# Kernel optimization log

Hardware: AMD Instinct MI355X
Metric: run time of the kernel (lower is better)

Reference implementation:

```python
import jax, jax.numpy as jnp
import numpy as np

H = 4                      # num_heads hard-coded in SDHGNN
NAMES = ["self", "cross", "self", "cross"]
POOL_SIZES = [2, 2, 2, 2]
MIN_NGHS = 128             # minium_nghs
EPS = 1e-3                 # InstanceNorm1d eps


def _pw(x, W, b):
    # pointwise Conv1d(kernel=1): [B, Cin, N] -> [B, Cout, N]
    return jnp.einsum('oi,bin->bon', W, x) + b[None, :, None]


def _instnorm(x):
    # InstanceNorm1d (no affine): normalize over N per (B, C)
    m = jnp.mean(x, axis=2, keepdims=True)
    v = jnp.mean((x - m) ** 2, axis=2, keepdims=True)
    return (x - m) * jax.lax.rsqrt(v + EPS)


def _attn_prop(x, src, p):
    # SharedAttentionalPropagation (sharing_attention=False):
    # MultiHeadedAttention + concat + MLP residual update.
    Wq, bq, Wk, bk, Wv, bv, Wm, bm, W1, b1, W2, b2 = p
    B, D, N = x.shape
    dh = D // H
    q = _pw(x, Wq, bq).reshape(B, dh, H, N)
    k = _pw(src, Wk, bk).reshape(B, dh, H, -1)
    v = _pw(src, Wv, bv).reshape(B, dh, H, -1)
    scores = jnp.einsum('bdhn,bdhm->bhnm', q, k) * (dh ** -0.5)
    prob = jax.nn.softmax(scores, axis=-1)                     # [B,H,N,M]
    msg = jnp.einsum('bhnm,bdhm->bdhn', prob, v).reshape(B, D, N)
    msg = _pw(msg, Wm, bm)
    y = jnp.concatenate([x, msg], axis=1)                      # [B,2D,N]
    h = jax.nn.relu(_instnorm(_pw(y, W1, b1)))
    return x + _pw(h, W2, b2), prob


def _gather(x, idx):
    # x: [B,D,N], idx: [B,K] -> [B,D,K]
    return jnp.take_along_axis(
        x, jnp.broadcast_to(idx[:, None, :], (x.shape[0], x.shape[1], idx.shape[1])), axis=2)


def _pool(prob, idx, pool_size):
    # pooling_by_prob (4-D prob branch): mean over heads, sum over queries,
    # top-k by importance, sorted indices, gather global indexes.
    K = idx.shape[1]
    p = prob.mean(axis=1).sum(axis=1)                          # [B,K]
    k = min(max(K // pool_size, MIN_NGHS), K)
    _, top = jax.lax.top_k(p, k)
    top = jnp.sort(top, axis=1)
    return jnp.take_along_axis(idx, top, axis=1)


def setup_inputs() -> dict:
    key = jax.random.key(0)
    B, D, N, L = 2, 128, 2048, 4
    ks = jax.random.split(key, 16)
    s = lambda fan: 1.0 / np.sqrt(fan)
    inp = {
        'x0': jax.random.normal(ks[0], (B, D, N), jnp.float32),
        'x1': jax.random.normal(ks[1], (B, D, N), jnp.float32),
        'Wq': jax.random.normal(ks[2], (L, D, D), jnp.float32) * s(D),
        'bq': jax.random.normal(ks[3], (L, D), jnp.float32) * 0.01,
        'Wk': jax.random.normal(ks[4], (L, D, D), jnp.float32) * s(D),
        'bk': jax.random.normal(ks[5], (L, D), jnp.float32) * 0.01,
        'Wv': jax.random.normal(ks[6], (L, D, D), jnp.float32) * s(D),
        'bv': jax.random.normal(ks[7], (L, D), jnp.float32) * 0.01,
        'Wm': jax.random.normal(ks[8], (L, D, D), jnp.float32) * s(D),
        'bm': jax.random.normal(ks[9], (L, D), jnp.float32) * 0.01,
        'W1': jax.random.normal(ks[10], (L, 2 * D, 2 * D), jnp.float32) * s(2 * D),
        'b1': jax.random.normal(ks[11], (L, 2 * D), jnp.float32) * 0.01,
        'W2': jax.random.normal(ks[12], (L, D, 2 * D), jnp.float32) * s(2 * D),
        'b2': jnp.zeros((L, D), jnp.float32),  # nn.init.constant_(mlp[-1].bias, 0)
    }
    return inp


def reference(x0, x1, Wq, bq, Wk, bk, Wv, bv, Wm, bm, W1, b1, W2, b2):
    B, D, N = x0.shape
    idx0 = jnp.broadcast_to(jnp.arange(N, dtype=jnp.int32)[None], (B, N))
    idx1 = idx0
    for l, (name, ps) in enumerate(zip(NAMES, POOL_SIZES)):
        p = (Wq[l], bq[l], Wk[l], bk[l], Wv[l], bv[l],
             Wm[l], bm[l], W1[l], b1[l], W2[l], b2[l])
        if name == 'self':
            s0, s1 = _gather(x0, idx0), _gather(x1, idx1)
        else:
            s0, s1 = _gather(x1, idx1), _gather(x0, idx0)
        x0, prob0 = _attn_prop(x0, s0, p)
        x1, prob1 = _attn_prop(x1, s1, p)
        if name == 'self':
            idx0 = _pool(prob0, idx0, ps)
            idx1 = _pool(prob1, idx1, ps)
        else:
            idx1 = _pool(prob0, idx1, ps)
            idx0 = _pool(prob1, idx0, ps)
    return jnp.stack([x0, x1], axis=0)   # [2, B, D, N]
```

## Files before the change

kernel.cpp:

```cpp
#include <hip/hip_runtime.h>
#include <cstdint>
#include <cstddef>


#define NB 2
#define ND 128
#define NH 4
#define NN 2048
#define ND2 256
#define DN (ND*NN)
#define BDN (NB*DN)
#define QK_SCALE 0.2550348623f
#define IN_EPS 1e-3f

typedef unsigned short u16;
typedef __attribute__((ext_vector_type(8))) short short8;
typedef __attribute__((ext_vector_type(4))) float f32x4;

__device__ __forceinline__ u16 f2bf(float f) {
    unsigned u = __float_as_uint(f);
    return (u16)((u + 0x7fffu + ((u >> 16) & 1u)) >> 16);
}
__device__ __forceinline__ float bf2f(u16 h) {
    return __uint_as_float(((unsigned)h) << 16);
}
__device__ __forceinline__ float fexp2(float x) {
#if __has_builtin(__builtin_amdgcn_exp2f)
    return __builtin_amdgcn_exp2f(x);
#else
    return exp2f(x);
#endif
}
__device__ __forceinline__ unsigned cvtpk_bf16(float a, float b) {
    unsigned r;
    asm("v_cvt_pk_bf16_f32 %0, %1, %2" : "=v"(r) : "v"(a), "v"(b));
    return r;
}

__global__ __launch_bounds__(256) void init_kernel(
    const float* __restrict__ x0in, const float* __restrict__ x1in,
    float* __restrict__ out, int* __restrict__ idx0, int* __restrict__ idx1)
{
    int tid = blockIdx.x * 256 + threadIdx.x;
    const float4* a = (const float4*)x0in;
    const float4* b = (const float4*)x1in;
    float4* o = (float4*)out;
    o[tid] = a[tid];
    o[BDN/4 + tid] = b[tid];
    if (tid < NB*NN) {
        int v = tid & (NN-1);
        idx0[tid] = v;
        idx1[tid] = v;
    }
}

__global__ __launch_bounds__(256) void wrepack2_kernel(
    const float* __restrict__ Wq, const float* __restrict__ Wk,
    const float* __restrict__ Wv, const float* __restrict__ Wm,
    const float* __restrict__ W1, const float* __restrict__ W2,
    const float* __restrict__ bq, const float* __restrict__ bk,
    const float* __restrict__ bv,
    u16* __restrict__ whi, u16* __restrict__ wlo,
    float* __restrict__ bqp, float* __restrict__ bkp, float* __restrict__ bvp)
{
    int e = blockIdx.x * 256 + threadIdx.x;
    if (e < 655360) {
        int l = e / 163840, r = e - l*163840;
        float v;
        if (r < 49152) {
            int m = r >> 14;
            int rr = r & 16383;
            int o = rr >> 7, c = rr & 127;
            int so = (o & 31)*4 + (o >> 5);
            const float* W = (m == 0) ? Wq : ((m == 1) ? Wk : Wv);
            v = W[l*16384 + so*128 + c];
        } else if (r < 65536) {
            int rr = r - 49152;
            int o = rr >> 7, c = rr & 127;
            int sc = (c & 31)*4 + (c >> 5);
            v = Wm[l*16384 + o*128 + sc];
        } else if (r < 131072) v = W1[l*65536 + r - 65536];
        else                   v = W2[l*32768 + r - 131072];
        u16 hb = f2bf(v);
        whi[e] = hb;
        wlo[e] = f2bf(v - bf2f(hb));
    } else if (e < 656896) {
        int eb = e - 655360;
        int l = eb / 384, rr = eb % 384;
        int which = rr >> 7, o = rr & 127;
        int so = (o & 31)*4 + (o >> 5);
        float v = (which == 0 ? bq : (which == 1 ? bk : bv))[l*128 + so];
        (which == 0 ? bqp : (which == 1 ? bkp : bvp))[l*128 + o] = v;
    }
}

__global__ __launch_bounds__(256) void repack_xh_kernel(
    const float* __restrict__ in, u16* __restrict__ ohi, u16* __restrict__ olo)
{
    __shared__ float tile[32][68];
    int z = blockIdx.y >> 2, cg = blockIdx.y & 3;
    int n0 = blockIdx.x * 64;
    int t = threadIdx.x;
    {
        int i = t >> 3, nc = (t & 7) * 8;
        const float* src = &in[((size_t)z*128 + cg*32 + i)*NN + n0 + nc];
        float4 a = *(const float4*)src;
        float4 b = *(const float4*)(src + 4);
        tile[i][nc+0]=a.x; tile[i][nc+1]=a.y; tile[i][nc+2]=a.z; tile[i][nc+3]=a.w;
        tile[i][nc+4]=b.x; tile[i][nc+5]=b.y; tile[i][nc+6]=b.z; tile[i][nc+7]=b.w;
    }
    __syncthreads();
    int n = t >> 2, c8 = (t & 3) * 8;
    short8 hi, lo;
    #pragma unroll
    for (int j = 0; j < 8; ++j) {
        float v = tile[c8 + j][n];
        u16 h = f2bf(v);
        hi[j] = (short)h;
        lo[j] = (short)f2bf(v - bf2f(h));
    }
    size_t ob = ((size_t)z*NN + n0 + n)*128 + cg*32 + c8;
    *(short8*)&ohi[ob] = hi;
    *(short8*)&olo[ob] = lo;
}

__device__ __forceinline__ void gcore(
    u16* As0, u16* As1, u16* Bs0, u16* Bs1,
    const u16* __restrict__ Whi, const u16* __restrict__ Wlo, int o0, int Cin,
    const u16* __restrict__ B1hi, const u16* __restrict__ B1lo, int s1,
    const u16* __restrict__ B2hi, const u16* __restrict__ B2lo, int s2, int split,
    size_t brow, int n0, const int* __restrict__ idxp, int t, f32x4 acc[2][2])
{
    const int lane = t & 63, w = t >> 6;
    const int l15 = lane & 15, quad = lane >> 4;
    const int wr = (w & 1)*32, wc = (w >> 1)*32;
    const int ao = t >> 2, ak = (t & 3)*8;
    int grow = n0 + ao;
    if (idxp) grow = idxp[grow];
    for (int kc = 0; kc < Cin; kc += 32) {
        {
            size_t wa = (size_t)(o0 + ao)*Cin + kc + ak;
            *(short8*)&As0[ao*40 + ak] = *(const short8*)&Whi[wa];
            *(short8*)&As1[ao*40 + ak] = *(const short8*)&Wlo[wa];
        }
        {
            int c = kc + ak;
            const u16 *ph, *pl;
            size_t off;
            if (c < split) { ph = B1hi; pl = B1lo; off = (brow + grow)*s1 + c; }
            else { ph = B2hi; pl = B2lo; off = (brow + grow)*s2 + (c - split); }
            *(short8*)&Bs0[ao*40 + ak] = *(const short8*)&ph[off];
            *(short8*)&Bs1[ao*40 + ak] = *(const short8*)&pl[off];
        }
        __syncthreads();
        short8 Ah[2], Al[2], Bh[2], Bl[2];
        #pragma unroll
        for (int a = 0; a < 2; ++a) {
            Ah[a] = *(const short8*)&As0[(wr + a*16 + l15)*40 + quad*8];
            Al[a] = *(const short8*)&As1[(wr + a*16 + l15)*40 + quad*8];
        }
        #pragma unroll
        for (int c = 0; c < 2; ++c) {
            Bh[c] = *(const short8*)&Bs0[(wc + c*16 + l15)*40 + quad*8];
            Bl[c] = *(const short8*)&Bs1[(wc + c*16 + l15)*40 + quad*8];
        }
        #pragma unroll
        for (int a = 0; a < 2; ++a)
            #pragma unroll
            for (int c = 0; c < 2; ++c) {
                acc[a][c] = __builtin_amdgcn_mfma_f32_16x16x32_bf16(Ah[a], Bl[c], acc[a][c], 0,0,0);
                acc[a][c] = __builtin_amdgcn_mfma_f32_16x16x32_bf16(Al[a], Bh[c], acc[a][c], 0,0,0);
                acc[a][c] = __builtin_amdgcn_mfma_f32_16x16x32_bf16(Ah[a], Bh[c], acc[a][c], 0,0,0);
            }
        __syncthreads();
    }
}

__global__ __launch_bounds__(256) void qkv_kernel(
    const u16* __restrict__ Whi, const u16* __restrict__ Wlo,
    const float* __restrict__ bqp, const float* __restrict__ bkp,
    const float* __restrict__ bvp,
    const u16* __restrict__ xphi, const u16* __restrict__ xplo,
    const int* __restrict__ idx0, const int* __restrict__ idx1,
    int cross, int M,
    u16* __restrict__ qthi, u16* __restrict__ qtlo,
    u16* __restrict__ kthi, u16* __restrict__ ktlo,
    u16* __restrict__ vthi, float* __restrict__ p)
{
    __shared__ u16 gsm[10240];
    u16* As0 = gsm;  u16* As1 = gsm + 2560;
    u16* Bs0 = gsm + 5120; u16* Bs1 = gsm + 7680;
    float* tb = (float*)gsm;

    const int z = blockIdx.z;
    const int bx = blockIdx.x;
    const int t = threadIdx.x;
    const int lane = t & 63, w = t >> 6;
    const int l15 = lane & 15, quad = lane >> 4;
    const int wr = (w & 1)*32, wc = (w >> 1)*32;

    int role, o0, n0, nCols;
    const u16 *Wbh, *Wbl;
    const float* bias;
    if (bx < 64) {
        role = 0; o0 = (bx & 1)*64; n0 = (bx >> 1)*64; nCols = NN;
        Wbh = Whi; Wbl = Wlo; bias = bqp;
        if (t < 32) p[(size_t)z*NN + bx*32 + t] = 0.f;
    } else {
        int e = bx - 64;
        int kt = M >> 6;
        int ct = e % kt, rt = e / kt;
        n0 = ct*64; nCols = M;
        if (rt < 2) { role = 1; o0 = rt*64; Wbh = Whi+16384; Wbl = Wlo+16384; bias = bkp; }
        else        { role = 2; o0 = (rt-2)*64; Wbh = Whi+32768; Wbl = Wlo+32768; bias = bvp; }
    }
    size_t brow = (size_t)z * NN;
    const int* idxp = nullptr;
    if (role != 0) {
        int ss = cross ? 1 - (z >> 1) : (z >> 1);
        brow = (size_t)(ss*2 + (z & 1)) * NN;
        idxp = (ss ? idx1 : idx0) + (z & 1)*NN;
    }

    f32x4 acc[2][2];
    #pragma unroll
    for (int a = 0; a < 2; ++a)
        #pragma unroll
        for (int c = 0; c < 2; ++c) acc[a][c] = (f32x4){0.f,0.f,0.f,0.f};

    gcore(As0, As1, Bs0, Bs1, Wbh, Wbl, o0, 128,
          xphi, xplo, 128, xphi, xplo, 128, 128, brow, n0, idxp, t, acc);

    if (role == 2) {
        #pragma unroll
        for (int a = 0; a < 2; ++a)
            #pragma unroll
            for (int c = 0; c < 2; ++c)
                #pragma unroll
                for (int r = 0; r < 4; ++r) {
                    int row = o0 + wr + a*16 + quad*4 + r;
                    int m = n0 + wc + c*16 + l15;
                    float v = acc[a][c][r] + bias[row];
                    vthi[((size_t)(z*4 + (row>>5))*32 + (row&31))*(size_t)M + m] = f2bf(v);
                }
    } else {
        float scale = role ? 1.f : QK_SCALE;
        #pragma unroll
        for (int a = 0; a < 2; ++a)
            #pragma unroll
            for (int c = 0; c < 2; ++c)
                #pragma unroll
                for (int r = 0; r < 4; ++r) {
                    int rl = wr + a*16 + quad*4 + r;
                    tb[rl*66 + wc + c*16 + l15] = acc[a][c][r] + bias[o0 + rl];
                }
        __syncthreads();
        u16* ohi = role ? kthi : qthi;
        u16* olo = role ? ktlo : qtlo;
        int n = t >> 2, rb = (t & 3)*16;
        #pragma unroll
        for (int g = 0; g < 2; ++g) {
            short8 hi, lo;
            #pragma unroll
            for (int j = 0; j < 8; ++j) {
                float v = tb[(rb + g*8 + j)*66 + n] * scale;
                u16 hb = f2bf(v);
                hi[j] = (short)hb;
                lo[j] = (short)f2bf(v - bf2f(hb));
            }
            int rowg = o0 + rb + g*8;
            size_t ob = ((size_t)(z*4 + (rowg >> 5))*nCols + n0 + n)*32 + (rowg & 31);
            *(short8*)&ohi[ob] = hi;
            *(short8*)&olo[ob] = lo;
        }
    }
}

__global__ __launch_bounds__(512, 6) void attn4_kernel(
    const u16* __restrict__ qthi, const u16* __restrict__ qtlo,
    const u16* __restrict__ kthi, const u16* __restrict__ ktlo,
    const u16* __restrict__ vthi, int M,
    u16* __restrict__ msghi, u16* __restrict__ msglo, float* __restrict__ p)
{
    __shared__ u16 kv[14592];
    __shared__ float pcol[2048];
    __shared__ float redm[4][64], redl[4][64];
    __shared__ float rowM[64], rowIV[64];

    u16* ks0 = kv;
    u16* ks1 = kv + 5120;
    u16* vs  = kv + 10240;
    float* obuf = (float*)kv;

    const int t = threadIdx.x;
    const int lane = t & 63, wave = t >> 6;
    const int l15 = lane & 15, quad = lane >> 4;
    const int qp = wave & 1, mh = wave >> 1;
    const int h = blockIdx.y, z = blockIdx.z;
    const int zh = z*4 + h;
    const int n0 = blockIdx.x * 64;

    for (int i = t; i < M; i += 512) pcol[i] = 0.f;

    short8 qBh[2], qBl[2];
    #pragma unroll
    for (int qt = 0; qt < 2; ++qt) {
        size_t qb = ((size_t)zh*NN + n0 + qp*32 + qt*16 + l15)*32 + quad*8;
        qBh[qt] = *(const short8*)&qthi[qb];
        qBl[qt] = *(const short8*)&qtlo[qb];
    }

    const int nch = M >> 7;
    const int sr = t >> 2, sc8 = (t & 3)*8;
    const int vr = t >> 4, vc8 = (t & 15)*8;

    float rm[2] = {-1e30f, -1e30f}, rl[2] = {0.f, 0.f};

    for (int ch = 0; ch < nch; ++ch) {
        const int m0 = ch << 7;
        {
            size_t gk = ((size_t)zh*M + m0 + sr)*32 + sc8;
            *(short8*)&ks0[sr*40 + sc8] = *(const short8*)&kthi[gk];
            *(short8*)&ks1[sr*40 + sc8] = *(const short8*)&ktlo[gk];
        }
        __syncthreads();
        #pragma unroll
        for (int qt = 0; qt < 2; ++qt)
            #pragma unroll
            for (int mt = 0; mt < 2; ++mt) {
                int mrow = mh*32 + mt*16 + l15;
                short8 kh = *(const short8*)&ks0[mrow*40 + quad*8];
                short8 kl = *(const short8*)&ks1[mrow*40 + quad*8];
                f32x4 a = {0.f,0.f,0.f,0.f};
                a = __builtin_amdgcn_mfma_f32_16x16x32_bf16(kh, qBl[qt], a, 0,0,0);
                a = __builtin_amdgcn_mfma_f32_16x16x32_bf16(kl, qBh[qt], a, 0,0,0);
                a = __builtin_amdgcn_mfma_f32_16x16x32_bf16(kh, qBh[qt], a, 0,0,0);
                float bm = fmaxf(fmaxf(a[0],a[1]), fmaxf(a[2],a[3]));
                float bs = fexp2(a[0]-bm)+fexp2(a[1]-bm)+fexp2(a[2]-bm)+fexp2(a[3]-bm);
                if (bm > rm[qt]) { rl[qt] = rl[qt]*fexp2(rm[qt]-bm) + bs; rm[qt] = bm; }
                else rl[qt] += bs*fexp2(bm - rm[qt]);
            }
        __syncthreads();
    }

    #pragma unroll
    for (int qt = 0; qt < 2; ++qt) {
        #pragma unroll
        for (int off = 16; off <= 32; off <<= 1) {
            float om = __shfl_xor(rm[qt], off);
            float ol = __shfl_xor(rl[qt], off);
            float nm = fmaxf(rm[qt], om);
            rl[qt] = rl[qt]*fexp2(rm[qt]-nm) + ol*fexp2(om-nm);
            rm[qt] = nm;
        }
        if (quad == 0) {
            redm[mh][qp*32 + qt*16 + l15] = rm[qt];
            redl[mh][qp*32 + qt*16 + l15] = rl[qt];
        }
    }
    __syncthreads();
    if (t < 64) {
        float m = redm[0][t], l = redl[0][t];
        #pragma unroll
        for (int w2 = 1; w2 < 4; ++w2) {
            float om = redm[w2][t];
            float nm = fmaxf(m, om);
            l = l*fexp2(m - nm) + redl[w2][t]*fexp2(om - nm);
            m = nm;
        }
        rowM[t] = m;
        rowIV[t] = 1.f / l;
    }
    __syncthreads();
    float myRM[2], myRIV[2];
    #pragma unroll
    for (int qt = 0; qt < 2; ++qt) {
        myRM[qt]  = rowM[qp*32 + qt*16 + l15];
        myRIV[qt] = rowIV[qp*32 + qt*16 + l15];
    }

    f32x4 oa[2][2];
    #pragma unroll
    for (int qt = 0; qt < 2; ++qt)
        #pragma unroll
        for (int dt = 0; dt < 2; ++dt) oa[qt][dt] = (f32x4){0.f,0.f,0.f,0.f};

    const int aA = (l15 + 32*(quad & 1))*4;
    const int aB = aA + 64;
    const bool mtsel = (quad >= 2);

    for (int ch = 0; ch < nch; ++ch) {
        const int m0 = ch << 7;
        {
            size_t gk = ((size_t)zh*M + m0 + sr)*32 + sc8;
            *(short8*)&ks0[sr*40 + sc8] = *(const short8*)&kthi[gk];
            *(short8*)&ks1[sr*40 + sc8] = *(const short8*)&ktlo[gk];
            *(short8*)&vs[vr*136 + vc8] =
                *(const short8*)&vthi[((size_t)zh*32 + vr)*M + m0 + vc8];
        }
        __syncthreads();

        float pr[2][2][4];
        #pragma unroll
        for (int qt = 0; qt < 2; ++qt)
            #pragma unroll
            for (int mt = 0; mt < 2; ++mt) {
                int mrow = mh*32 + mt*16 + l15;
                short8 kh = *(const short8*)&ks0[mrow*40 + quad*8];
                short8 kl = *(const short8*)&ks1[mrow*40 + quad*8];
                f32x4 a = {0.f,0.f,0.f,0.f};
                a = __builtin_amdgcn_mfma_f32_16x16x32_bf16(kh, qBl[qt], a, 0,0,0);
                a = __builtin_amdgcn_mfma_f32_16x16x32_bf16(kl, qBh[qt], a, 0,0,0);
                a = __builtin_amdgcn_mfma_f32_16x16x32_bf16(kh, qBh[qt], a, 0,0,0);
                #pragma unroll
                for (int r = 0; r < 4; ++r)
                    pr[qt][mt][r] = fexp2(a[r] - myRM[qt]);
            }

        #pragma unroll
        for (int mt = 0; mt < 2; ++mt)
            #pragma unroll
            for (int r = 0; r < 4; ++r) {
                float ps = pr[0][mt][r]*myRIV[0] + pr[1][mt][r]*myRIV[1];
                ps += __shfl_xor(ps, 1);
                ps += __shfl_xor(ps, 2);
                ps += __shfl_xor(ps, 4);
                ps += __shfl_xor(ps, 8);
                if (l15 == 0)
                    atomicAdd(&pcol[m0 + mh*32 + mt*16 + quad*4 + r], ps);
            }

        short8 vA[2];
        #pragma unroll
        for (int dt = 0; dt < 2; ++dt)
            vA[dt] = *(const short8*)&vs[(dt*16 + l15)*136 + mh*32 + quad*8];

        #pragma unroll
        for (int qt = 0; qt < 2; ++qt) {
            unsigned pk00 = cvtpk_bf16(pr[qt][0][0], pr[qt][0][1]);
            unsigned pk01 = cvtpk_bf16(pr[qt][0][2], pr[qt][0][3]);
            unsigned pk10 = cvtpk_bf16(pr[qt][1][0], pr[qt][1][1]);
            unsigned pk11 = cvtpk_bf16(pr[qt][1][2], pr[qt][1][3]);
            unsigned a0 = (unsigned)__builtin_amdgcn_ds_bpermute(aA, (int)pk00);
            unsigned a1 = (unsigned)__builtin_amdgcn_ds_bpermute(aA, (int)pk01);
            unsigned a2 = (unsigned)__builtin_amdgcn_ds_bpermute(aA, (int)pk10);
            unsigned a3 = (unsigned)__builtin_amdgcn_ds_bpermute(aA, (int)pk11);
            unsigned b0 = (unsigned)__builtin_amdgcn_ds_bpermute(aB, (int)pk00);
            unsigned b1 = (unsigned)__builtin_amdgcn_ds_bpermute(aB, (int)pk01);
            unsigned b2 = (unsigned)__builtin_amdgcn_ds_bpermute(aB, (int)pk10);
            unsigned b3 = (unsigned)__builtin_amdgcn_ds_bpermute(aB, (int)pk11);
            union { unsigned u[4]; short8 s; } fb;
            fb.u[0] = mtsel ? a2 : a0;
            fb.u[1] = mtsel ? a3 : a1;
            fb.u[2] = mtsel ? b2 : b0;
            fb.u[3] = mtsel ? b3 : b1;
            #pragma unroll
            for (int dt = 0; dt < 2; ++dt)
                oa[qt][dt] = __builtin_amdgcn_mfma_f32_16x16x32_bf16(vA[dt], fb.s, oa[qt][dt], 0,0,0);
        }
        __syncthreads();
    }

    if (mh > 0) {
        #pragma unroll
        for (int qt = 0; qt < 2; ++qt)
            #pragma unroll
            for (int dt = 0; dt < 2; ++dt)
                #pragma unroll
                for (int r = 0; r < 4; ++r) {
                    int q = qp*32 + qt*16 + l15;
                    int d = dt*16 + quad*4 + r;
                    obuf[((mh-1)*32 + d)*66 + q] = oa[qt][dt][r];
                }
    }
    __syncthreads();
    if (mh == 0) {
        #pragma unroll
        for (int qt = 0; qt < 2; ++qt)
            #pragma unroll
            for (int dt = 0; dt < 2; ++dt)
                #pragma unroll
                for (int r = 0; r < 4; ++r) {
                    int q = qp*32 + qt*16 + l15;
                    int d = dt*16 + quad*4 + r;
                    float v = oa[qt][dt][r];
                    #pragma unroll
                    for (int w2 = 0; w2 < 3; ++w2)
                        v += obuf[(w2*32 + d)*66 + q];
                    obuf[d*66 + q] = v * myRIV[qt];
                }
    }
    __syncthreads();
    {
        int tt = t & 255;
        int n = tt >> 2, i8 = (tt & 3)*8;
        short8 o8;
        if (t < 256) {
            #pragma unroll
            for (int j = 0; j < 8; ++j) o8[j] = (short)f2bf(obuf[(i8+j)*66 + n]);
            *(short8*)&msghi[((size_t)z*NN + n0 + n)*128 + h*32 + i8] = o8;
        } else {
            #pragma unroll
            for (int j = 0; j < 8; ++j) {
                float v = obuf[(i8+j)*66 + n];
                u16 hb = f2bf(v);
                o8[j] = (short)f2bf(v - bf2f(hb));
            }
            *(short8*)&msglo[((size_t)z*NN + n0 + n)*128 + h*32 + i8] = o8;
        }
    }
    for (int i = t; i < M; i += 512)
        atomicAdd(&p[(size_t)z*NN + i], pcol[i]*0.25f);
}

__global__ __launch_bounds__(256) void wm_kernel(
    const u16* __restrict__ Wmh, const u16* __restrict__ Wml,
    const float* __restrict__ bm,
    const u16* __restrict__ msghi, const u16* __restrict__ msglo,
    u16* __restrict__ m2hi, u16* __restrict__ m2lo,
    float* __restrict__ gsum, float* __restrict__ gsq)
{
    __shared__ u16 gsm[10240];
    u16* As0 = gsm;  u16* As1 = gsm + 2560;
    u16* Bs0 = gsm + 5120; u16* Bs1 = gsm + 7680;
    float* tb = (float*)gsm;

    const int z = blockIdx.z, o0 = blockIdx.y*64, n0 = blockIdx.x*64;
    const int t = threadIdx.x;
    const int lane = t & 63, w = t >> 6;
    const int l15 = lane & 15, quad = lane >> 4;
    const int wr = (w & 1)*32, wc = (w >> 1)*32;

    if (blockIdx.x == 0 && blockIdx.y == 0) {
        gsum[z*256 + t] = 0.f;
        gsq[z*256 + t] = 0.f;
    }

    f32x4 acc[2][2];
    #pragma unroll
    for (int a = 0; a < 2; ++a)
        #pragma unroll
        for (int c = 0; c < 2; ++c) acc[a][c] = (f32x4){0.f,0.f,0.f,0.f};
    gcore(As0, As1, Bs0, Bs1, Wmh, Wml, o0, 128,
          msghi, msglo, 128, msghi, msglo, 128, 128,
          (size_t)z*NN, n0, nullptr, t, acc);

    #pragma unroll
    for (int a = 0; a < 2; ++a)
        #pragma unroll
        for (int c = 0; c < 2; ++c)
            #pragma unroll
            for (int r = 0; r < 4; ++r) {
                int rl = wr + a*16 + quad*4 + r;
                tb[rl*66 + wc + c*16 + l15] = acc[a][c][r] + bm[o0 + rl];
            }
    __syncthreads();
    int n = t >> 2, rb = (t & 3)*16;
    #pragma unroll
    for (int g = 0; g < 2; ++g) {
        short8 hi, lo;
        #pragma unroll
        for (int j = 0; j < 8; ++j) {
            float v = tb[(rb + g*8 + j)*66 + n];
            u16 hb = f2bf(v);
            hi[j] = (short)hb;
            lo[j] = (short)f2bf(v - bf2f(hb));
        }
        size_t ob = ((size_t)z*NN + n0 + n)*128 + o0 + rb + g*8;
        *(short8*)&m2hi[ob] = hi;
        *(short8*)&m2lo[ob] = lo;
    }
}

__global__ __launch_bounds__(256) void w1_kernel(
    const u16* __restrict__ W1h, const u16* __restrict__ W1l,
    const float* __restrict__ b1,
    const u16* __restrict__ xphi, const u16* __restrict__ xplo,
    const u16* __restrict__ m2hi, const u16* __restrict__ m2lo,
    float* __restrict__ zf, float* __restrict__ gsum, float* __restrict__ gsq)
{
    __shared__ u16 gsm[10240];
    u16* As0 = gsm;  u16* As1 = gsm + 2560;
    u16* Bs0 = gsm + 5120; u16* Bs1 = gsm + 7680;

    const int z = blockIdx.z, o0 = blockIdx.y*64, n0 = blockIdx.x*64;
    const int t = threadIdx.x;
    const int lane = t & 63, w = t >> 6;
    const int l15 = lane & 15, quad = lane >> 4;
    const int wr = (w & 1)*32, wc = (w >> 1)*32;

    f32x4 acc[2][2];
    #pragma unroll
    for (int a = 0; a < 2; ++a)
        #pragma unroll
        for (int c = 0; c < 2; ++c) acc[a][c] = (f32x4){0.f,0.f,0.f,0.f};
    gcore(As0, As1, Bs0, Bs1, W1h, W1l, o0, 256,
          xphi, xplo, 128, m2hi, m2lo, 128, 128,
          (size_t)z*NN, n0, nullptr, t, acc);

    float ssum[2][4], ssq[2][4];
    #pragma unroll
    for (int a = 0; a < 2; ++a)
        #pragma unroll
        for (int r = 0; r < 4; ++r) { ssum[a][r] = 0.f; ssq[a][r] = 0.f; }
    #pragma unroll
    for (int a = 0; a < 2; ++a)
        #pragma unroll
        for (int c = 0; c < 2; ++c)
            #pragma unroll
            for (int r = 0; r < 4; ++r) {
                int row = o0 + wr + a*16 + quad*4 + r;
                int n = n0 + wc + c*16 + l15;
                float v = acc[a][c][r] + b1[row];
                zf[((size_t)z*256 + row)*NN + n] = v;
                ssum[a][r] += v;
                ssq[a][r] = fmaf(v, v, ssq[a][r]);
            }
    #pragma unroll
    for (int a = 0; a < 2; ++a)
        #pragma unroll
        for (int r = 0; r < 4; ++r) {
            float s = ssum[a][r], q2 = ssq[a][r];
            #pragma unroll
            for (int o = 1; o < 16; o <<= 1) {
                s  += __shfl_xor(s, o);
                q2 += __shfl_xor(q2, o);
            }
            if (l15 == 0) {
                int row = o0 + wr + a*16 + quad*4 + r;
                atomicAdd(&gsum[z*256 + row], s);
                atomicAdd(&gsq[z*256 + row], q2);
            }
        }
}

__global__ __launch_bounds__(256) void hrepack_kernel(
    const float* __restrict__ zf, const float* __restrict__ gsum,
    const float* __restrict__ gsq, u16* __restrict__ hhi, u16* __restrict__ hlo)
{
    __shared__ float tile[32][68];
    int z = blockIdx.y >> 3, cg = blockIdx.y & 7;
    int n0 = blockIdx.x * 64;
    int t = threadIdx.x;
    {
        int i = t >> 3, nc = (t & 7) * 8;
        int c = cg*32 + i;
        float mean = gsum[z*256 + c] * (1.f/NN);
        float var = gsq[z*256 + c] * (1.f/NN) - mean*mean;
        float iv = rsqrtf(var + IN_EPS);
        const float* src = &zf[((size_t)z*256 + c)*NN + n0 + nc];
        float4 a = *(const float4*)src;
        float4 b = *(const float4*)(src + 4);
        float vv[8] = {a.x,a.y,a.z,a.w,b.x,b.y,b.z,b.w};
        #pragma unroll
        for (int j = 0; j < 8; ++j) {
            float v = (vv[j] - mean) * iv;
            tile[i][nc + j] = v > 0.f ? v : 0.f;
        }
    }
    __syncthreads();
    int n = t >> 2, c8 = (t & 3) * 8;
    short8 hi, lo;
    #pragma unroll
    for (int j = 0; j < 8; ++j) {
        float v = tile[c8 + j][n];
        u16 hb = f2bf(v);
        hi[j] = (short)hb;
        lo[j] = (short)f2bf(v - bf2f(hb));
    }
    size_t ob = ((size_t)z*NN + n0 + n)*256 + cg*32 + c8;
    *(short8*)&hhi[ob] = hi;
    *(short8*)&hlo[ob] = lo;
}

__global__ __launch_bounds__(256) void w2_kernel(
    const u16* __restrict__ W2h, const u16* __restrict__ W2l,
    const float* __restrict__ b2,
    const u16* __restrict__ hhi, const u16* __restrict__ hlo,
    float* __restrict__ out, u16* __restrict__ xphi, u16* __restrict__ xplo,
    int writeplanes)
{
    __shared__ u16 gsm[10240];
    u16* As0 = gsm;  u16* As1 = gsm + 2560;
    u16* Bs0 = gsm + 5120; u16* Bs1 = gsm + 7680;
    float* tb = (float*)gsm;

    const int z = blockIdx.z, o0 = blockIdx.y*64, n0 = blockIdx.x*64;
    const int t = threadIdx.x;
    const int lane = t & 63, w = t >> 6;
    const int l15 = lane & 15, quad = lane >> 4;
    const int wr = (w & 1)*32, wc = (w >> 1)*32;

    f32x4 acc[2][2];
    #pragma unroll
    for (int a = 0; a < 2; ++a)
        #pragma unroll
        for (int c = 0; c < 2; ++c) acc[a][c] = (f32x4){0.f,0.f,0.f,0.f};
    gcore(As0, As1, Bs0, Bs1, W2h, W2l, o0, 256,
          hhi, hlo, 256, hhi, hlo, 256, 256,
          (size_t)z*NN, n0, nullptr, t, acc);

    #pragma unroll
    for (int a = 0; a < 2; ++a)
        #pragma unroll
        for (int c = 0; c < 2; ++c)
            #pragma unroll
            for (int r = 0; r < 4; ++r) {
                int rl = wr + a*16 + quad*4 + r;
                int rowg = o0 + rl;
                int n = n0 + wc + c*16 + l15;
                size_t oi = ((size_t)z*128 + rowg)*NN + n;
                float v = acc[a][c][r] + b2[rowg] + out[oi];
                out[oi] = v;
                tb[rl*66 + wc + c*16 + l15] = v;
            }
    __syncthreads();
    if (writeplanes) {
        int n = t >> 2, rb = (t & 3)*16;
        #pragma unroll
        for (int g = 0; g < 2; ++g) {
            short8 hi, lo;
            #pragma unroll
            for (int j = 0; j < 8; ++j) {
                float v = tb[(rb + g*8 + j)*66 + n];
                u16 hb = f2bf(v);
                hi[j] = (short)hb;
                lo[j] = (short)f2bf(v - bf2f(hb));
            }
            size_t ob = ((size_t)z*NN + n0 + n)*128 + o0 + rb + g*8;
            *(short8*)&xphi[ob] = hi;
            *(short8*)&xplo[ob] = lo;
        }
    }
}

__global__ __launch_bounds__(256) void rank_kernel(
    const float* __restrict__ p, int* __restrict__ rank, int M)
{
    int zz = blockIdx.y;
    __shared__ float pv[2048];
    for (int i = threadIdx.x; i < M; i += 256) pv[i] = p[(size_t)zz*NN + i];
    __syncthreads();
    int i = blockIdx.x * 256 + threadIdx.x;
    if (i < M) {
        float pi = pv[i];
        int r = 0;
        for (int j = 0; j < M; ++j) {
            float pj = pv[j];
            r += (pj > pi) ? 1 : ((pj == pi && j < i) ? 1 : 0);
        }
        rank[zz*NN + i] = r;
    }
}

__global__ __launch_bounds__(256) void select_kernel(
    const int* __restrict__ rank, int* __restrict__ idx0, int* __restrict__ idx1,
    int M, int k, int cross)
{
    int z = blockIdx.x;
    int st = z >> 1, b = z & 1;
    int ts = cross ? 1 - st : st;
    int* idx = (ts ? idx1 : idx0) + b * NN;
    const int* rk = rank + z * NN;
    __shared__ int sel[2048], idv[2048], sa[2048], sb[2048];
    int t = threadIdx.x;
    for (int i = t; i < M; i += 256) {
        int s = rk[i] < k ? 1 : 0;
        sel[i] = s;
        sa[i] = s;
        idv[i] = idx[i];
    }
    __syncthreads();
    int* src = sa; int* dst = sb;
    for (int off = 1; off < M; off <<= 1) {
        for (int i = t; i < M; i += 256)
            dst[i] = src[i] + (i >= off ? src[i - off] : 0);
        __syncthreads();
        int* tmp = src; src = dst; dst = tmp;
    }
    for (int i = t; i < M; i += 256)
        if (sel[i]) idx[src[i] - 1] = idv[i];
}

extern "C" void kernel_launch(void* const* d_in, const int* in_sizes, int n_in,
                              void* d_out, int out_size, void* d_ws, size_t ws_size,
                              hipStream_t stream)
{
    const float* x0in = (const float*)d_in[0];
    const float* x1in = (const float*)d_in[1];
    const float* Wq = (const float*)d_in[2];
    const float* bq = (const float*)d_in[3];
    const float* Wk = (const float*)d_in[4];
    const float* bk = (const float*)d_in[5];
    const float* Wv = (const float*)d_in[6];
    const float* bv = (const float*)d_in[7];
    const float* Wm = (const float*)d_in[8];
    const float* bm = (const float*)d_in[9];
    const float* W1 = (const float*)d_in[10];
    const float* b1 = (const float*)d_in[11];
    const float* W2 = (const float*)d_in[12];
    const float* b2 = (const float*)d_in[13];

    float* out = (float*)d_out;
    float* ws  = (float*)d_ws;

    const size_t U = 1048576;
    u16* ub   = (u16*)ws;
    u16* xphi = ub;            u16* xplo = ub + U;
    u16* qthi = ub + 2*U;      u16* qtlo = ub + 3*U;
    u16* kthi = ub + 4*U;      u16* ktlo = ub + 5*U;
    u16* vthi = ub + 6*U;
    u16* msghi = ub + 7*U;     u16* msglo = ub + 8*U;
    u16* m2hi = ub + 9*U;      u16* m2lo = ub + 10*U;
    u16* hhi  = ub + 11*U;     u16* hlo = ub + 13*U;
    u16* whi  = ub + 15*U;     u16* wlo = whi + 655360;
    float* zf = (float*)(ub + 2*U);
    float* ft = (float*)(wlo + 655360);
    float* bqp = ft;           float* bkp = ft + 512;      float* bvp = ft + 1024;
    float* gsum = ft + 1536;   float* gsq = ft + 2560;
    float* p = ft + 3584;
    int* idx0 = (int*)(p + 4*NN);
    int* idx1 = idx0 + NB*NN;
    int* rankb = idx1 + NB*NN;

    init_kernel<<<BDN/4/256, 256, 0, stream>>>(x0in, x1in, out, idx0, idx1);
    wrepack2_kernel<<<2566, 256, 0, stream>>>(Wq, Wk, Wv, Wm, W1, W2, bq, bk, bv,
                                              whi, wlo, bqp, bkp, bvp);
    repack_xh_kernel<<<dim3(32, 16), 256, 0, stream>>>(out, xphi, xplo);

    const int Ms[4] = {2048, 1024, 512, 256};
    for (int l = 0; l < 4; ++l) {
        int M = Ms[l];
        int k_new = (M/2 < 128) ? 128 : M/2;
        int cross = l & 1;
        size_t lw = (size_t)l * 163840;
        const u16* Wlh = whi + lw;  const u16* Wll = wlo + lw;

        qkv_kernel<<<dim3(64 + 4*(M/64), 1, 4), 256, 0, stream>>>(
            Wlh, Wll, bqp + l*128, bkp + l*128, bvp + l*128,
            xphi, xplo, idx0, idx1, cross, M,
            qthi, qtlo, kthi, ktlo, vthi, p);

        attn4_kernel<<<dim3(32, NH, 4), 512, 0, stream>>>(
            qthi, qtlo, kthi, ktlo, vthi, M, msghi, msglo, p);

        wm_kernel<<<dim3(32, 2, 4), 256, 0, stream>>>(
            Wlh + 49152, Wll + 49152, bm + l*128,
            msghi, msglo, m2hi, m2lo, gsum, gsq);

        w1_kernel<<<dim3(32, 4, 4), 256, 0, stream>>>(
            Wlh + 65536, Wll + 65536, b1 + l*256,
            xphi, xplo, m2hi, m2lo, zf, gsum, gsq);

        hrepack_kernel<<<dim3(32, 32), 256, 0, stream>>>(zf, gsum, gsq, hhi, hlo);

        w2_kernel<<<dim3(32, 2, 4), 256, 0, stream>>>(
            Wlh + 131072, Wll + 131072, b2 + l*128,
            hhi, hlo, out, xphi, xplo, (l < 3) ? 1 : 0);

        rank_kernel<<<dim3((M+255)/256, 4), 256, 0, stream>>>(p, rankb, M);
        select_kernel<<<4, 256, 0, stream>>>(rankb, idx0, idx1, M, k_new, cross);
    }
}
```

Before: 567.4 us.

## Register-prefetch next tile global loads in GEMM core and attention loops

The GEMM core and both attention passes now load the next K/V (or weight/activation) tile from global memory into registers while the current tile is being computed, then store it to shared memory at the top of the next iteration. The aim is to hide global load latency behind the MFMA work, and the barrier placement is reworked to suit this. The attention kernel's minimum-occupancy hint drops from 6 to 4 blocks to leave room for the extra prefetch registers. The cost is more register pressure and lower occupancy.

```diff
diff --git a/kernel.cpp b/kernel.cpp
--- a/kernel.cpp
+++ b/kernel.cpp
@@ -137,20 +137,35 @@
     const int ao = t >> 2, ak = (t & 3)*8;
     int grow = n0 + ao;
     if (idxp) grow = idxp[grow];
+
+    short8 rA0, rA1, rB0, rB1;
+    {
+        size_t wa = (size_t)(o0 + ao)*Cin + ak;
+        rA0 = *(const short8*)&Whi[wa];
+        rA1 = *(const short8*)&Wlo[wa];
+        int c = ak;
+        const u16 *ph, *pl; size_t off;
+        if (c < split) { ph = B1hi; pl = B1lo; off = (brow + grow)*s1 + c; }
+        else { ph = B2hi; pl = B2lo; off = (brow + grow)*s2 + (c - split); }
+        rB0 = *(const short8*)&ph[off];
+        rB1 = *(const short8*)&pl[off];
+    }
     for (int kc = 0; kc < Cin; kc += 32) {
-        {
-            size_t wa = (size_t)(o0 + ao)*Cin + kc + ak;
-            *(short8*)&As0[ao*40 + ak] = *(const short8*)&Whi[wa];
-            *(short8*)&As1[ao*40 + ak] = *(const short8*)&Wlo[wa];
-        }
-        {
-            int c = kc + ak;
-            const u16 *ph, *pl;
-            size_t off;
+        __syncthreads();
+        *(short8*)&As0[ao*40 + ak] = rA0;
+        *(short8*)&As1[ao*40 + ak] = rA1;
+        *(short8*)&Bs0[ao*40 + ak] = rB0;
+        *(short8*)&Bs1[ao*40 + ak] = rB1;
+        if (kc + 32 < Cin) {
+            size_t wa = (size_t)(o0 + ao)*Cin + kc + 32 + ak;
+            rA0 = *(const short8*)&Whi[wa];
+            rA1 = *(const short8*)&Wlo[wa];
+            int c = kc + 32 + ak;
+            const u16 *ph, *pl; size_t off;
             if (c < split) { ph = B1hi; pl = B1lo; off = (brow + grow)*s1 + c; }
             else { ph = B2hi; pl = B2lo; off = (brow + grow)*s2 + (c - split); }
-            *(short8*)&Bs0[ao*40 + ak] = *(const short8*)&ph[off];
-            *(short8*)&Bs1[ao*40 + ak] = *(const short8*)&pl[off];
+            rB0 = *(const short8*)&ph[off];
+            rB1 = *(const short8*)&pl[off];
         }
         __syncthreads();
         short8 Ah[2], Al[2], Bh[2], Bl[2];
@@ -172,8 +187,8 @@
                 acc[a][c] = __builtin_amdgcn_mfma_f32_16x16x32_bf16(Al[a], Bh[c], acc[a][c], 0,0,0);
                 acc[a][c] = __builtin_amdgcn_mfma_f32_16x16x32_bf16(Ah[a], Bh[c], acc[a][c], 0,0,0);
             }
-        __syncthreads();
-    }
+    }
+    __syncthreads();
 }
 
 __global__ __launch_bounds__(256) void qkv_kernel(
@@ -276,7 +291,7 @@
     }
 }
 
-__global__ __launch_bounds__(512, 6) void attn4_kernel(
+__global__ __launch_bounds__(512, 4) void attn4_kernel(
     const u16* __restrict__ qthi, const u16* __restrict__ qtlo,
     const u16* __restrict__ kthi, const u16* __restrict__ ktlo,
     const u16* __restrict__ vthi, int M,
@@ -316,12 +331,21 @@
 
     float rm[2] = {-1e30f, -1e30f}, rl[2] = {0.f, 0.f};
 
+    short8 skh, skl, sv;
+    {
+        size_t gk = ((size_t)zh*M + sr)*32 + sc8;
+        skh = *(const short8*)&kthi[gk];
+        skl = *(const short8*)&ktlo[gk];
+    }
+
     for (int ch = 0; ch < nch; ++ch) {
-        const int m0 = ch << 7;
-        {
-            size_t gk = ((size_t)zh*M + m0 + sr)*32 + sc8;
-            *(short8*)&ks0[sr*40 + sc8] = *(const short8*)&kthi[gk];
-            *(short8*)&ks1[sr*40 + sc8] = *(const short8*)&ktlo[gk];
+        __syncthreads();
+        *(short8*)&ks0[sr*40 + sc8] = skh;
+        *(short8*)&ks1[sr*40 + sc8] = skl;
+        if (ch + 1 < nch) {
+            size_t gk = ((size_t)zh*M + ((ch+1) << 7) + sr)*32 + sc8;
+            skh = *(const short8*)&kthi[gk];
+            skl = *(const short8*)&ktlo[gk];
         }
         __syncthreads();
         #pragma unroll
@@ -340,7 +364,13 @@
                 if (bm > rm[qt]) { rl[qt] = rl[qt]*fexp2(rm[qt]-bm) + bs; rm[qt] = bm; }
                 else rl[qt] += bs*fexp2(bm - rm[qt]);
             }
-        __syncthreads();
+    }
+
+    {
+        size_t gk = ((size_t)zh*M + sr)*32 + sc8;
+        skh = *(const short8*)&kthi[gk];
+        skl = *(const short8*)&ktlo[gk];
+        sv  = *(const short8*)&vthi[((size_t)zh*32 + vr)*M + vc8];
     }
 
     #pragma unroll
@@ -391,12 +421,16 @@
 
     for (int ch = 0; ch < nch; ++ch) {
         const int m0 = ch << 7;
-        {
-            size_t gk = ((size_t)zh*M + m0 + sr)*32 + sc8;
-            *(short8*)&ks0[sr*40 + sc8] = *(const short8*)&kthi[gk];
-            *(short8*)&ks1[sr*40 + sc8] = *(const short8*)&ktlo[gk];
-            *(short8*)&vs[vr*136 + vc8] =
-                *(const short8*)&vthi[((size_t)zh*32 + vr)*M + m0 + vc8];
+        __syncthreads();
+        *(short8*)&ks0[sr*40 + sc8] = skh;
+        *(short8*)&ks1[sr*40 + sc8] = skl;
+        *(short8*)&vs[vr*136 + vc8] = sv;
+        if (ch + 1 < nch) {
+            int m1 = (ch+1) << 7;
+            size_t gk = ((size_t)zh*M + m1 + sr)*32 + sc8;
+            skh = *(const short8*)&kthi[gk];
+            skl = *(const short8*)&ktlo[gk];
+            sv  = *(const short8*)&vthi[((size_t)zh*32 + vr)*M + m1 + vc8];
         }
         __syncthreads();
 
@@ -458,8 +492,8 @@
             for (int dt = 0; dt < 2; ++dt)
                 oa[qt][dt] = __builtin_amdgcn_mfma_f32_16x16x32_bf16(vA[dt], fb.s, oa[qt][dt], 0,0,0);
         }
-        __syncthreads();
-    }
+    }
+    __syncthreads();
 
     if (mh > 0) {
         #pragma unroll
```

Measured after the change: 542.3 us. 1.05x faster.
